# Optimization experiments

Measured on AMD Instinct MI355X. Metric: run time of the kernel, lower is better.

## Reference

```python
import jax, jax.numpy as jnp
import numpy as np

D_MODEL, D_FF, N_EXPERTS, TOP_K = 1024, 4096, 8, 2


def setup_inputs() -> dict:
    key = jax.random.key(0)
    ks = jax.random.split(key, 7)
    s = 0.02
    return {
        "x": jax.random.normal(ks[0], (2, 2048, D_MODEL), dtype=jnp.float32),
        "router_w": jax.random.normal(ks[1], (D_MODEL, N_EXPERTS), dtype=jnp.float32) * s,
        "router_b": jnp.zeros((N_EXPERTS,), dtype=jnp.float32),
        "w1": jax.random.normal(ks[2], (N_EXPERTS, D_MODEL, D_FF), dtype=jnp.float32) * s,
        "b1": jnp.zeros((N_EXPERTS, D_FF), dtype=jnp.float32),
        "w2": jax.random.normal(ks[3], (N_EXPERTS, D_FF, D_MODEL), dtype=jnp.float32) * s,
        "b2": jnp.zeros((N_EXPERTS, D_MODEL), dtype=jnp.float32),
    }


def reference(x, router_w, router_b, w1, b1, w2, b2):
    bsz, seq_len, d_model = x.shape
    flat_x = x.reshape(-1, d_model)                      # [T, D]
    logits = flat_x @ router_w + router_b                # [T, E]
    topk_scores, topk_idx = jax.lax.top_k(logits, TOP_K) # [T, K]
    gates = jax.nn.softmax(topk_scores, axis=-1).astype(flat_x.dtype)
    mixed = jnp.zeros_like(flat_x)
    num_experts = w1.shape[0]
    for e in range(num_experts):
        # dense per-expert MLP over all tokens; tokens not routed to e get weight 0,
        # so the math matches the original gather-MLP-scatter exactly.
        h = jax.nn.gelu(flat_x @ w1[e] + b1[e], approximate=False)  # exact GELU as torch nn.GELU
        y = h @ w2[e] + b2[e]                                       # [T, D]
        w_e = jnp.sum(jnp.where(topk_idx == e, gates, 0.0), axis=-1, keepdims=True)  # [T, 1]
        mixed = mixed + w_e * y
    return mixed.reshape(bsz, seq_len, d_model)
```

## Files before the change

kernel.cpp:

```cpp
#include <hip/hip_runtime.h>
#include <hip/hip_bf16.h>
#include <stdint.h>

#define T_TOK 4096
#define DM 1024
#define DF 4096
#define NE 8
#define PADROWS 10240

typedef __attribute__((ext_vector_type(8))) short short8;
typedef __attribute__((ext_vector_type(8))) unsigned short ushort8_t;
typedef __attribute__((ext_vector_type(4))) float f32x4;

__device__ __forceinline__ unsigned short f2bf(float f) {
    union { float f; unsigned u; } v; v.f = f;
    unsigned r = v.u + 0x7fffu + ((v.u >> 16) & 1u);
    return (unsigned short)(r >> 16);
}

__device__ __forceinline__ void async_cp16(const void* g, void* l) {
    __builtin_amdgcn_global_load_lds(
        (const __attribute__((address_space(1))) unsigned*)g,
        (__attribute__((address_space(3))) unsigned*)l,
        16, 0, 0);
}

__global__ __launch_bounds__(256) void k_router(
    const float* __restrict__ x, const float* __restrict__ rw,
    const float* __restrict__ rb, int* __restrict__ counts,
    int* __restrict__ listTok, int4* __restrict__ tokRec,
    float2* __restrict__ tokGate)
{
    int l  = threadIdx.x & 63;
    int wv = threadIdx.x >> 6;
    int t  = blockIdx.x * 4 + wv;
    const float* xr = x + (size_t)t * DM;
    float acc[NE];
#pragma unroll
    for (int e = 0; e < NE; ++e) acc[e] = 0.f;
#pragma unroll
    for (int i = 0; i < 16; ++i) {
        int d = i * 64 + l;
        float xv = xr[d];
        const float4* wp = (const float4*)(rw + (size_t)d * NE);
        float4 w0 = wp[0], w1 = wp[1];
        acc[0] += xv * w0.x; acc[1] += xv * w0.y; acc[2] += xv * w0.z; acc[3] += xv * w0.w;
        acc[4] += xv * w1.x; acc[5] += xv * w1.y; acc[6] += xv * w1.z; acc[7] += xv * w1.w;
    }
#pragma unroll
    for (int off = 32; off >= 1; off >>= 1)
#pragma unroll
        for (int e = 0; e < NE; ++e) acc[e] += __shfl_down(acc[e], off);
    if (l == 0) {
        float lg[NE];
#pragma unroll
        for (int e = 0; e < NE; ++e) lg[e] = acc[e] + rb[e];
        int i1 = 0; float s1 = lg[0];
#pragma unroll
        for (int e = 1; e < NE; ++e) if (lg[e] > s1) { s1 = lg[e]; i1 = e; }
        int i2 = -1; float s2 = -3.0e38f;
#pragma unroll
        for (int e = 0; e < NE; ++e) if (e != i1 && lg[e] > s2) { s2 = lg[e]; i2 = e; }
        float g1 = 1.f / (1.f + expf(s2 - s1));
        float g2 = 1.f - g1;
        int p1 = atomicAdd(&counts[i1], 1);
        listTok[i1 * T_TOK + p1] = t;
        int p2 = atomicAdd(&counts[i2], 1);
        listTok[i2 * T_TOK + p2] = t;
        tokRec[t]  = make_int4(i1, p1, i2, p2);
        tokGate[t] = make_float2(g1, g2);
    }
}

__global__ void k_offsets(const int* __restrict__ counts, int* __restrict__ offsets)
{
    int cum = 0;
    for (int e = 0; e < NE; ++e) { offsets[e] = cum; cum += (counts[e] + 255) & ~255; }
    offsets[NE] = cum;
}

__global__ __launch_bounds__(256) void k_packw(const float* __restrict__ src,
                                               unsigned short* __restrict__ dst,
                                               int K, int N)
{
    __shared__ float tile[64][65];
    int e  = blockIdx.z;
    int n0 = blockIdx.x * 64;
    int k0 = blockIdx.y * 64;
    const float* s    = src + (size_t)e * K * N;
    unsigned short* d = dst + (size_t)e * K * N;
    int tid = threadIdx.x;
#pragma unroll
    for (int i = 0; i < 4; ++i) {
        int u  = i * 256 + tid;
        int kk = u >> 4;
        int nn = (u & 15) * 4;
        float4 v = *(const float4*)(s + (size_t)(k0 + kk) * N + n0 + nn);
        tile[kk][nn] = v.x; tile[kk][nn + 1] = v.y; tile[kk][nn + 2] = v.z; tile[kk][nn + 3] = v.w;
    }
    __syncthreads();
#pragma unroll
    for (int i = 0; i < 4; ++i) {
        int u  = i * 256 + tid;
        int nn = u >> 4;
        int g  = (u >> 1) & 7;
        int h  = (u & 1) * 4;
        int kc = g * 8 + h;
        int n  = n0 + nn;
        ushort4 o;
        o.x = f2bf(tile[kc + 0][nn]); o.y = f2bf(tile[kc + 1][nn]);
        o.z = f2bf(tile[kc + 2][nn]); o.w = f2bf(tile[kc + 3][nn]);
        int gp = g ^ (n & 7);
        size_t off = ((size_t)(k0 >> 6) * N + n) * 64 + gp * 8 + h;
        *(ushort4*)(d + off) = o;
    }
}

__global__ __launch_bounds__(256) void k_packa(
    const float* __restrict__ x, const int* __restrict__ listTok,
    const int* __restrict__ counts, const int* __restrict__ offsets,
    unsigned short* __restrict__ ap)
{
    int r0  = blockIdx.x * 64;
    int kt  = blockIdx.y;
    int tid = threadIdx.x;
    __shared__ int toks[64];
    if (tid < 64) {
        int r = r0 + tid;
        int tok = 0;
        int total = offsets[NE];
        if (r < total) {
            int e = 0;
#pragma unroll
            for (int j = 1; j < NE; ++j) if (r >= offsets[j]) e = j;
            int local = r - offsets[e];
            int c = counts[e];
            if (local >= c) local = c - 1;
            if (local < 0) local = 0;
            tok = (c > 0) ? listTok[e * T_TOK + local] : 0;
        }
        toks[tid] = tok;
    }
    __syncthreads();
#pragma unroll
    for (int i = 0; i < 4; ++i) {
        int u  = i * 256 + tid;
        int rl = u >> 4;
        int g  = (u >> 1) & 7;
        int h  = (u & 1) * 4;
        int tok = toks[rl];
        float4 v = *(const float4*)(x + (size_t)tok * DM + kt * 64 + g * 8 + h);
        ushort4 o; o.x = f2bf(v.x); o.y = f2bf(v.y); o.z = f2bf(v.z); o.w = f2bf(v.w);
        int row = r0 + rl;
        int gp  = g ^ (row & 7);
        size_t off = ((size_t)kt * PADROWS + row) * 64 + gp * 8 + h;
        *(ushort4*)(ap + off) = o;
    }
}

__global__ __launch_bounds__(256) void k_ffn1(
    const unsigned short* __restrict__ ap, const unsigned short* __restrict__ w1p,
    const float* __restrict__ b1, const int* __restrict__ counts,
    const int* __restrict__ offsets, unsigned short* __restrict__ Hp)
{
    __shared__ __align__(16) unsigned short lsA[128 * 64];
    __shared__ __align__(16) unsigned short lsB[128 * 64];
    int i  = blockIdx.x;
    int e  = i & 7;
    int j  = i >> 3;
    int mt = j & 31;
    int y  = j >> 5;
    int cnt = counts[e];
    int m0  = mt << 7;
    if (m0 >= cnt) return;
    int hbase = offsets[e];
    int n0    = y << 7;
    int tid = threadIdx.x, wv = tid >> 6, l = tid & 63;
    int wm = wv & 1, wn = wv >> 1;

    const unsigned short* srcA = ap + ((size_t)hbase + m0) * 64;
    const unsigned short* srcB = w1p + (size_t)e * DM * DF;

    f32x4 acc[4][4];
#pragma unroll
    for (int a = 0; a < 4; ++a)
#pragma unroll
        for (int b = 0; b < 4; ++b) acc[a][b] = (f32x4)(0.f);

    for (int kt = 0; kt < 16; ++kt) {
        const unsigned short* gA = srcA + (size_t)kt * PADROWS * 64;
        const unsigned short* gB = srcB + ((size_t)kt * DF + n0) * 64;
#pragma unroll
        for (int jj = 0; jj < 4; ++jj) {
            int c = (wv * 4 + jj) * 512;
            async_cp16(gA + c + l * 8, lsA + c);
            async_cp16(gB + c + l * 8, lsB + c);
        }
        __syncthreads();
#pragma unroll
        for (int ks = 0; ks < 2; ++ks) {
            short8 aF[4], bF[4];
#pragma unroll
            for (int mi = 0; mi < 4; ++mi) {
                int row = wm * 64 + mi * 16 + (l & 15);
                int g   = ks * 4 + (l >> 4);
                aF[mi] = *(const short8*)&lsA[row * 64 + ((g ^ (row & 7)) << 3)];
            }
#pragma unroll
            for (int ni = 0; ni < 4; ++ni) {
                int row = wn * 64 + ni * 16 + (l & 15);
                int g   = ks * 4 + (l >> 4);
                bF[ni] = *(const short8*)&lsB[row * 64 + ((g ^ (row & 7)) << 3)];
            }
#pragma unroll
            for (int mi = 0; mi < 4; ++mi)
#pragma unroll
                for (int ni = 0; ni < 4; ++ni)
                    acc[mi][ni] = __builtin_amdgcn_mfma_f32_16x16x32_bf16(aF[mi], bF[ni], acc[mi][ni], 0, 0, 0);
        }
        __syncthreads();
    }

    int q = l >> 4, cn = l & 15;
#pragma unroll
    for (int mi = 0; mi < 4; ++mi) {
#pragma unroll
        for (int ni = 0; ni < 4; ++ni) {
            int nloc = wn * 64 + ni * 16 + cn;
            float bias = b1[e * DF + n0 + nloc];
            unsigned short* base = (nloc & 64) ? lsB : lsA;
            int kc = nloc & 63, g = kc >> 3;
#pragma unroll
            for (int rg = 0; rg < 4; ++rg) {
                int m = wm * 64 + mi * 16 + q * 4 + rg;
                float v = acc[mi][ni][rg] + bias;
                v = 0.5f * v * (1.f + erff(v * 0.70710678118f));
                int gp = g ^ (m & 7);
                base[m * 64 + gp * 8 + (kc & 7)] = f2bf(v);
            }
        }
    }
    __syncthreads();
    {
        int c = tid >> 7;
        int r = tid & 127;
        const unsigned short* s = (c ? lsB : lsA) + r * 64;
        unsigned short* dst = Hp + (((size_t)(n0 >> 6) + c) * PADROWS + hbase + m0 + r) * 64;
#pragma unroll
        for (int jj = 0; jj < 8; ++jj)
            *(ushort8_t*)(dst + jj * 8) = *(const ushort8_t*)(s + jj * 8);
    }
}

__global__ __launch_bounds__(256) void k_ffn2(
    const unsigned short* __restrict__ Hp, const unsigned short* __restrict__ w2p,
    const float* __restrict__ b2, const int* __restrict__ counts,
    const int* __restrict__ offsets, float* __restrict__ ypart)
{
    __shared__ __align__(16) unsigned short lsA[128 * 64];
    __shared__ __align__(16) unsigned short lsB[128 * 64];
    int i  = blockIdx.x;
    int e  = i & 7;
    int j  = i >> 3;
    int mt = j & 31;
    int y  = j >> 5;
    int cnt = counts[e];
    int m0  = mt << 7;
    if (m0 >= cnt) return;
    int R0 = offsets[e] + m0;
    int n0 = y << 7;
    int tid = threadIdx.x, wv = tid >> 6, l = tid & 63;
    int wm = wv & 1, wn = wv >> 1;

    const unsigned short* srcA = Hp + (size_t)R0 * 64;
    const unsigned short* srcB = w2p + (size_t)e * DF * DM;

    f32x4 acc[4][4];
#pragma unroll
    for (int a = 0; a < 4; ++a)
#pragma unroll
        for (int b = 0; b < 4; ++b) acc[a][b] = (f32x4)(0.f);

    for (int kt = 0; kt < 64; ++kt) {
        const unsigned short* gA = srcA + (size_t)kt * PADROWS * 64;
        const unsigned short* gB = srcB + ((size_t)kt * DM + n0) * 64;
#pragma unroll
        for (int jj = 0; jj < 4; ++jj) {
            int c = (wv * 4 + jj) * 512;
            async_cp16(gA + c + l * 8, lsA + c);
            async_cp16(gB + c + l * 8, lsB + c);
        }
        __syncthreads();
#pragma unroll
        for (int ks = 0; ks < 2; ++ks) {
            short8 aF[4], bF[4];
#pragma unroll
            for (int mi = 0; mi < 4; ++mi) {
                int row = wm * 64 + mi * 16 + (l & 15);
                int g   = ks * 4 + (l >> 4);
                aF[mi] = *(const short8*)&lsA[row * 64 + ((g ^ (row & 7)) << 3)];
            }
#pragma unroll
            for (int ni = 0; ni < 4; ++ni) {
                int row = wn * 64 + ni * 16 + (l & 15);
                int g   = ks * 4 + (l >> 4);
                bF[ni] = *(const short8*)&lsB[row * 64 + ((g ^ (row & 7)) << 3)];
            }
#pragma unroll
            for (int mi = 0; mi < 4; ++mi)
#pragma unroll
                for (int ni = 0; ni < 4; ++ni)
                    acc[mi][ni] = __builtin_amdgcn_mfma_f32_16x16x32_bf16(aF[mi], bF[ni], acc[mi][ni], 0, 0, 0);
        }
        __syncthreads();
    }

    int q = l >> 4, cn = l & 15;
    float bias[4];
#pragma unroll
    for (int ni = 0; ni < 4; ++ni) bias[ni] = b2[e * DM + n0 + wn * 64 + ni * 16 + cn];
#pragma unroll
    for (int mi = 0; mi < 4; ++mi) {
#pragma unroll
        for (int rg = 0; rg < 4; ++rg) {
            int m = wm * 64 + mi * 16 + q * 4 + rg;
            float* orow = ypart + ((size_t)R0 + m) * DM;
#pragma unroll
            for (int ni = 0; ni < 4; ++ni)
                orow[n0 + wn * 64 + ni * 16 + cn] = acc[mi][ni][rg] + bias[ni];
        }
    }
}

__global__ __launch_bounds__(256) void k_gather(
    const float* __restrict__ yp, const int4* __restrict__ rec,
    const float2* __restrict__ gg, const int* __restrict__ offsets,
    float* __restrict__ out)
{
    int t = blockIdx.x;
    int4 rc = rec[t];
    float2 w = gg[t];
    size_t r1 = (size_t)offsets[rc.x] + rc.y;
    size_t r2 = (size_t)offsets[rc.z] + rc.w;
    const float4* a = (const float4*)(yp + r1 * DM);
    const float4* b = (const float4*)(yp + r2 * DM);
    float4 va = a[threadIdx.x], vb = b[threadIdx.x];
    float4 o;
    o.x = w.x * va.x + w.y * vb.x;
    o.y = w.x * va.y + w.y * vb.y;
    o.z = w.x * va.z + w.y * vb.z;
    o.w = w.x * va.w + w.y * vb.w;
    ((float4*)(out + (size_t)t * DM))[threadIdx.x] = o;
}

extern "C" void kernel_launch(void* const* d_in, const int* in_sizes, int n_in,
                              void* d_out, int out_size, void* d_ws, size_t ws_size,
                              hipStream_t stream)
{
    const float* x  = (const float*)d_in[0];
    const float* rw = (const float*)d_in[1];
    const float* rb = (const float*)d_in[2];
    const float* w1 = (const float*)d_in[3];
    const float* b1 = (const float*)d_in[4];
    const float* w2 = (const float*)d_in[5];
    const float* b2 = (const float*)d_in[6];
    float* out = (float*)d_out;

    char* ws = (char*)d_ws;
    int*            counts   = (int*)(ws + 0);
    int*            offsets  = (int*)(ws + 128);
    int*            listTok  = (int*)(ws + 512);
    unsigned short* apack    = (unsigned short*)(ws + 262656);
    unsigned short* w2p      = (unsigned short*)(ws + 262656);
    unsigned short* w1p      = (unsigned short*)(ws + 21234176);
    unsigned short* Hp       = (unsigned short*)(ws + 88343040);
    float*          ypart    = (float*)(ws + 172229120);
    int4*           tokRec   = (int4*)(ws + 214172160);
    float2*         tokGate  = (float2*)(ws + 214237696);

    hipMemsetAsync(counts, 0, 32, stream);

    k_router <<<T_TOK / 4, 256, 0, stream>>>(x, rw, rb, counts, listTok, tokRec, tokGate);
    k_offsets<<<1, 1, 0, stream>>>(counts, offsets);
    k_packw  <<<dim3(DF / 64, DM / 64, NE), 256, 0, stream>>>(w1, w1p, DM, DF);
    k_packa  <<<dim3(PADROWS / 64, 16), 256, 0, stream>>>(x, listTok, counts, offsets, apack);
    k_ffn1   <<<NE * 32 * 32, 256, 0, stream>>>(apack, w1p, b1, counts, offsets, Hp);
    k_packw  <<<dim3(DM / 64, DF / 64, NE), 256, 0, stream>>>(w2, w2p, DF, DM);
    k_ffn2   <<<NE * 32 * 8, 256, 0, stream>>>(Hp, w2p, b2, counts, offsets, ypart);
    k_gather <<<T_TOK, 256, 0, stream>>>(ypart, tokRec, tokGate, offsets, out);
}
```

Baseline: 652.7 us.

## Use persistent atomic work-queue scheduling for both expert FFN GEMMs

Both grouped GEMM kernels become persistent: a fixed grid of 1280 blocks pulls tiles from a global atomic counter instead of launching one block per possible tile. Tile order also changes so that, for a given N column, all experts and M tiles come first, which may improve weight and activation reuse in L2. Empty tiles for experts with few tokens are skipped cheaply without the cost of launching a block for each. The price is one extra atomic and barrier per tile, and the counters now depend on the enlarged memset at the start of each launch.

```diff
diff --git a/kernel.cpp b/kernel.cpp
--- a/kernel.cpp
+++ b/kernel.cpp
@@ -161,173 +161,189 @@
 __global__ __launch_bounds__(256) void k_ffn1(
     const unsigned short* __restrict__ ap, const unsigned short* __restrict__ w1p,
     const float* __restrict__ b1, const int* __restrict__ counts,
-    const int* __restrict__ offsets, unsigned short* __restrict__ Hp)
+    const int* __restrict__ offsets, unsigned short* __restrict__ Hp,
+    int* __restrict__ wctr)
 {
     __shared__ __align__(16) unsigned short lsA[128 * 64];
     __shared__ __align__(16) unsigned short lsB[128 * 64];
-    int i  = blockIdx.x;
-    int e  = i & 7;
-    int j  = i >> 3;
-    int mt = j & 31;
-    int y  = j >> 5;
-    int cnt = counts[e];
-    int m0  = mt << 7;
-    if (m0 >= cnt) return;
-    int hbase = offsets[e];
-    int n0    = y << 7;
+    __shared__ int s_w;
     int tid = threadIdx.x, wv = tid >> 6, l = tid & 63;
     int wm = wv & 1, wn = wv >> 1;
 
-    const unsigned short* srcA = ap + ((size_t)hbase + m0) * 64;
-    const unsigned short* srcB = w1p + (size_t)e * DM * DF;
-
-    f32x4 acc[4][4];
-#pragma unroll
-    for (int a = 0; a < 4; ++a)
-#pragma unroll
-        for (int b = 0; b < 4; ++b) acc[a][b] = (f32x4)(0.f);
-
-    for (int kt = 0; kt < 16; ++kt) {
-        const unsigned short* gA = srcA + (size_t)kt * PADROWS * 64;
-        const unsigned short* gB = srcB + ((size_t)kt * DF + n0) * 64;
-#pragma unroll
-        for (int jj = 0; jj < 4; ++jj) {
-            int c = (wv * 4 + jj) * 512;
-            async_cp16(gA + c + l * 8, lsA + c);
-            async_cp16(gB + c + l * 8, lsB + c);
-        }
+    while (true) {
         __syncthreads();
-#pragma unroll
-        for (int ks = 0; ks < 2; ++ks) {
-            short8 aF[4], bF[4];
-#pragma unroll
-            for (int mi = 0; mi < 4; ++mi) {
-                int row = wm * 64 + mi * 16 + (l & 15);
-                int g   = ks * 4 + (l >> 4);
-                aF[mi] = *(const short8*)&lsA[row * 64 + ((g ^ (row & 7)) << 3)];
-            }
+        if (tid == 0) s_w = atomicAdd(wctr, 1);
+        __syncthreads();
+        int w = s_w;
+        if (w >= 8192) break;
+        int y  = w >> 8;
+        int e  = (w >> 5) & 7;
+        int mt = w & 31;
+        int cnt = counts[e];
+        int m0  = mt << 7;
+        if (m0 >= cnt) continue;
+        int hbase = offsets[e];
+        int n0    = y << 7;
+
+        const unsigned short* srcA = ap + ((size_t)hbase + m0) * 64;
+        const unsigned short* srcB = w1p + (size_t)e * DM * DF;
+
+        f32x4 acc[4][4];
+#pragma unroll
+        for (int a = 0; a < 4; ++a)
+#pragma unroll
+            for (int b = 0; b < 4; ++b) acc[a][b] = (f32x4)(0.f);
+
+        for (int kt = 0; kt < 16; ++kt) {
+            const unsigned short* gA = srcA + (size_t)kt * PADROWS * 64;
+            const unsigned short* gB = srcB + ((size_t)kt * DF + n0) * 64;
+#pragma unroll
+            for (int jj = 0; jj < 4; ++jj) {
+                int c = (wv * 4 + jj) * 512;
+                async_cp16(gA + c + l * 8, lsA + c);
+                async_cp16(gB + c + l * 8, lsB + c);
+            }
+            __syncthreads();
+#pragma unroll
+            for (int ks = 0; ks < 2; ++ks) {
+                short8 aF[4], bF[4];
+#pragma unroll
+                for (int mi = 0; mi < 4; ++mi) {
+                    int row = wm * 64 + mi * 16 + (l & 15);
+                    int g   = ks * 4 + (l >> 4);
+                    aF[mi] = *(const short8*)&lsA[row * 64 + ((g ^ (row & 7)) << 3)];
+                }
+#pragma unroll
+                for (int ni = 0; ni < 4; ++ni) {
+                    int row = wn * 64 + ni * 16 + (l & 15);
+                    int g   = ks * 4 + (l >> 4);
+                    bF[ni] = *(const short8*)&lsB[row * 64 + ((g ^ (row & 7)) << 3)];
+                }
+#pragma unroll
+                for (int mi = 0; mi < 4; ++mi)
+#pragma unroll
+                    for (int ni = 0; ni < 4; ++ni)
+                        acc[mi][ni] = __builtin_amdgcn_mfma_f32_16x16x32_bf16(aF[mi], bF[ni], acc[mi][ni], 0, 0, 0);
+            }
+            __syncthreads();
+        }
+
+        int q = l >> 4, cn = l & 15;
+#pragma unroll
+        for (int mi = 0; mi < 4; ++mi) {
 #pragma unroll
             for (int ni = 0; ni < 4; ++ni) {
-                int row = wn * 64 + ni * 16 + (l & 15);
-                int g   = ks * 4 + (l >> 4);
-                bF[ni] = *(const short8*)&lsB[row * 64 + ((g ^ (row & 7)) << 3)];
-            }
-#pragma unroll
-            for (int mi = 0; mi < 4; ++mi)
-#pragma unroll
-                for (int ni = 0; ni < 4; ++ni)
-                    acc[mi][ni] = __builtin_amdgcn_mfma_f32_16x16x32_bf16(aF[mi], bF[ni], acc[mi][ni], 0, 0, 0);
+                int nloc = wn * 64 + ni * 16 + cn;
+                float bias = b1[e * DF + n0 + nloc];
+                unsigned short* base = (nloc & 64) ? lsB : lsA;
+                int kc = nloc & 63, g = kc >> 3;
+#pragma unroll
+                for (int rg = 0; rg < 4; ++rg) {
+                    int m = wm * 64 + mi * 16 + q * 4 + rg;
+                    float v = acc[mi][ni][rg] + bias;
+                    v = 0.5f * v * (1.f + erff(v * 0.70710678118f));
+                    int gp = g ^ (m & 7);
+                    base[m * 64 + gp * 8 + (kc & 7)] = f2bf(v);
+                }
+            }
         }
         __syncthreads();
-    }
-
-    int q = l >> 4, cn = l & 15;
-#pragma unroll
-    for (int mi = 0; mi < 4; ++mi) {
-#pragma unroll
-        for (int ni = 0; ni < 4; ++ni) {
-            int nloc = wn * 64 + ni * 16 + cn;
-            float bias = b1[e * DF + n0 + nloc];
-            unsigned short* base = (nloc & 64) ? lsB : lsA;
-            int kc = nloc & 63, g = kc >> 3;
-#pragma unroll
-            for (int rg = 0; rg < 4; ++rg) {
-                int m = wm * 64 + mi * 16 + q * 4 + rg;
-                float v = acc[mi][ni][rg] + bias;
-                v = 0.5f * v * (1.f + erff(v * 0.70710678118f));
-                int gp = g ^ (m & 7);
-                base[m * 64 + gp * 8 + (kc & 7)] = f2bf(v);
-            }
-        }
-    }
-    __syncthreads();
-    {
-        int c = tid >> 7;
-        int r = tid & 127;
-        const unsigned short* s = (c ? lsB : lsA) + r * 64;
-        unsigned short* dst = Hp + (((size_t)(n0 >> 6) + c) * PADROWS + hbase + m0 + r) * 64;
-#pragma unroll
-        for (int jj = 0; jj < 8; ++jj)
-            *(ushort8_t*)(dst + jj * 8) = *(const ushort8_t*)(s + jj * 8);
+        {
+            int c = tid >> 7;
+            int r = tid & 127;
+            const unsigned short* s = (c ? lsB : lsA) + r * 64;
+            unsigned short* dst = Hp + (((size_t)(n0 >> 6) + c) * PADROWS + hbase + m0 + r) * 64;
+#pragma unroll
+            for (int jj = 0; jj < 8; ++jj)
+                *(ushort8_t*)(dst + jj * 8) = *(const ushort8_t*)(s + jj * 8);
+        }
     }
 }
 
 __global__ __launch_bounds__(256) void k_ffn2(
     const unsigned short* __restrict__ Hp, const unsigned short* __restrict__ w2p,
     const float* __restrict__ b2, const int* __restrict__ counts,
-    const int* __restrict__ offsets, float* __restrict__ ypart)
+    const int* __restrict__ offsets, float* __restrict__ ypart,
+    int* __restrict__ wctr)
 {
     __shared__ __align__(16) unsigned short lsA[128 * 64];
     __shared__ __align__(16) unsigned short lsB[128 * 64];
-    int i  = blockIdx.x;
-    int e  = i & 7;
-    int j  = i >> 3;
-    int mt = j & 31;
-    int y  = j >> 5;
-    int cnt = counts[e];
-    int m0  = mt << 7;
-    if (m0 >= cnt) return;
-    int R0 = offsets[e] + m0;
-    int n0 = y << 7;
+    __shared__ int s_w;
     int tid = threadIdx.x, wv = tid >> 6, l = tid & 63;
     int wm = wv & 1, wn = wv >> 1;
 
-    const unsigned short* srcA = Hp + (size_t)R0 * 64;
-    const unsigned short* srcB = w2p + (size_t)e * DF * DM;
-
-    f32x4 acc[4][4];
-#pragma unroll
-    for (int a = 0; a < 4; ++a)
-#pragma unroll
-        for (int b = 0; b < 4; ++b) acc[a][b] = (f32x4)(0.f);
-
-    for (int kt = 0; kt < 64; ++kt) {
-        const unsigned short* gA = srcA + (size_t)kt * PADROWS * 64;
-        const unsigned short* gB = srcB + ((size_t)kt * DM + n0) * 64;
-#pragma unroll
-        for (int jj = 0; jj < 4; ++jj) {
-            int c = (wv * 4 + jj) * 512;
-            async_cp16(gA + c + l * 8, lsA + c);
-            async_cp16(gB + c + l * 8, lsB + c);
-        }
+    while (true) {
         __syncthreads();
-#pragma unroll
-        for (int ks = 0; ks < 2; ++ks) {
-            short8 aF[4], bF[4];
-#pragma unroll
-            for (int mi = 0; mi < 4; ++mi) {
-                int row = wm * 64 + mi * 16 + (l & 15);
-                int g   = ks * 4 + (l >> 4);
-                aF[mi] = *(const short8*)&lsA[row * 64 + ((g ^ (row & 7)) << 3)];
-            }
-#pragma unroll
-            for (int ni = 0; ni < 4; ++ni) {
-                int row = wn * 64 + ni * 16 + (l & 15);
-                int g   = ks * 4 + (l >> 4);
-                bF[ni] = *(const short8*)&lsB[row * 64 + ((g ^ (row & 7)) << 3)];
-            }
-#pragma unroll
-            for (int mi = 0; mi < 4; ++mi)
+        if (tid == 0) s_w = atomicAdd(wctr, 1);
+        __syncthreads();
+        int w = s_w;
+        if (w >= 2048) break;
+        int y  = w >> 8;
+        int e  = (w >> 5) & 7;
+        int mt = w & 31;
+        int cnt = counts[e];
+        int m0  = mt << 7;
+        if (m0 >= cnt) continue;
+        int R0 = offsets[e] + m0;
+        int n0 = y << 7;
+
+        const unsigned short* srcA = Hp + (size_t)R0 * 64;
+        const unsigned short* srcB = w2p + (size_t)e * DF * DM;
+
+        f32x4 acc[4][4];
+#pragma unroll
+        for (int a = 0; a < 4; ++a)
+#pragma unroll
+            for (int b = 0; b < 4; ++b) acc[a][b] = (f32x4)(0.f);
+
+        for (int kt = 0; kt < 64; ++kt) {
+            const unsigned short* gA = srcA + (size_t)kt * PADROWS * 64;
+            const unsigned short* gB = srcB + ((size_t)kt * DM + n0) * 64;
+#pragma unroll
+            for (int jj = 0; jj < 4; ++jj) {
+                int c = (wv * 4 + jj) * 512;
+                async_cp16(gA + c + l * 8, lsA + c);
+                async_cp16(gB + c + l * 8, lsB + c);
+            }
+            __syncthreads();
+#pragma unroll
+            for (int ks = 0; ks < 2; ++ks) {
+                short8 aF[4], bF[4];
+#pragma unroll
+                for (int mi = 0; mi < 4; ++mi) {
+                    int row = wm * 64 + mi * 16 + (l & 15);
+                    int g   = ks * 4 + (l >> 4);
+                    aF[mi] = *(const short8*)&lsA[row * 64 + ((g ^ (row & 7)) << 3)];
+                }
+#pragma unroll
+                for (int ni = 0; ni < 4; ++ni) {
+                    int row = wn * 64 + ni * 16 + (l & 15);
+                    int g   = ks * 4 + (l >> 4);
+                    bF[ni] = *(const short8*)&lsB[row * 64 + ((g ^ (row & 7)) << 3)];
+                }
+#pragma unroll
+                for (int mi = 0; mi < 4; ++mi)
+#pragma unroll
+                    for (int ni = 0; ni < 4; ++ni)
+                        acc[mi][ni] = __builtin_amdgcn_mfma_f32_16x16x32_bf16(aF[mi], bF[ni], acc[mi][ni], 0, 0, 0);
+            }
+            __syncthreads();
+        }
+
+        int q = l >> 4, cn = l & 15;
+        float bias[4];
+#pragma unroll
+        for (int ni = 0; ni < 4; ++ni) bias[ni] = b2[e * DM + n0 + wn * 64 + ni * 16 + cn];
+#pragma unroll
+        for (int mi = 0; mi < 4; ++mi) {
+#pragma unroll
+            for (int rg = 0; rg < 4; ++rg) {
+                int m = wm * 64 + mi * 16 + q * 4 + rg;
+                float* orow = ypart + ((size_t)R0 + m) * DM;
 #pragma unroll
                 for (int ni = 0; ni < 4; ++ni)
-                    acc[mi][ni] = __builtin_amdgcn_mfma_f32_16x16x32_bf16(aF[mi], bF[ni], acc[mi][ni], 0, 0, 0);
-        }
-        __syncthreads();
-    }
-
-    int q = l >> 4, cn = l & 15;
-    float bias[4];
-#pragma unroll
-    for (int ni = 0; ni < 4; ++ni) bias[ni] = b2[e * DM + n0 + wn * 64 + ni * 16 + cn];
-#pragma unroll
-    for (int mi = 0; mi < 4; ++mi) {
-#pragma unroll
-        for (int rg = 0; rg < 4; ++rg) {
-            int m = wm * 64 + mi * 16 + q * 4 + rg;
-            float* orow = ypart + ((size_t)R0 + m) * DM;
-#pragma unroll
-            for (int ni = 0; ni < 4; ++ni)
-                orow[n0 + wn * 64 + ni * 16 + cn] = acc[mi][ni][rg] + bias[ni];
+                    orow[n0 + wn * 64 + ni * 16 + cn] = acc[mi][ni][rg] + bias[ni];
+            }
         }
     }
 }
@@ -368,6 +384,8 @@
 
     char* ws = (char*)d_ws;
     int*            counts   = (int*)(ws + 0);
+    int*            wctr1    = (int*)(ws + 64);
+    int*            wctr2    = (int*)(ws + 68);
     int*            offsets  = (int*)(ws + 128);
     int*            listTok  = (int*)(ws + 512);
     unsigned short* apack    = (unsigned short*)(ws + 262656);
@@ -378,14 +396,14 @@
     int4*           tokRec   = (int4*)(ws + 214172160);
     float2*         tokGate  = (float2*)(ws + 214237696);
 
-    hipMemsetAsync(counts, 0, 32, stream);
+    hipMemsetAsync(ws, 0, 128, stream);
 
     k_router <<<T_TOK / 4, 256, 0, stream>>>(x, rw, rb, counts, listTok, tokRec, tokGate);
     k_offsets<<<1, 1, 0, stream>>>(counts, offsets);
     k_packw  <<<dim3(DF / 64, DM / 64, NE), 256, 0, stream>>>(w1, w1p, DM, DF);
     k_packa  <<<dim3(PADROWS / 64, 16), 256, 0, stream>>>(x, listTok, counts, offsets, apack);
-    k_ffn1   <<<NE * 32 * 32, 256, 0, stream>>>(apack, w1p, b1, counts, offsets, Hp);
+    k_ffn1   <<<1280, 256, 0, stream>>>(apack, w1p, b1, counts, offsets, Hp, wctr1);
     k_packw  <<<dim3(DM / 64, DF / 64, NE), 256, 0, stream>>>(w2, w2p, DF, DM);
-    k_ffn2   <<<NE * 32 * 8, 256, 0, stream>>>(Hp, w2p, b2, counts, offsets, ypart);
+    k_ffn2   <<<1280, 256, 0, stream>>>(Hp, w2p, b2, counts, offsets, ypart, wctr2);
     k_gather <<<T_TOK, 256, 0, stream>>>(ypart, tokRec, tokGate, offsets, out);
 }
```

Result: slower. 755.1 us (+15.7%).
